# Optimization experiments

Hardware: AMD Instinct MI355X
Metric: run time of the kernel (lower is better)

The kernel has to match this reference:

```python
import jax, jax.numpy as jnp
import numpy as np
from jax import lax


def _conv(x, w, b=None):
    # NCHW conv, 'same' padding, stride 1
    y = lax.conv_general_dilated(x, w, (1, 1), 'SAME',
                                 dimension_numbers=('NCHW', 'OIHW', 'NCHW'))
    return y if b is None else y + b[None, :, None, None]


def _up2(x):
    # nn.Upsample(scale_factor=2), nearest
    return jnp.repeat(jnp.repeat(x, 2, axis=2), 2, axis=3)


def _rot_attn(x, wq, wk, wv, lng, lnb, reach=1):
    # Batched sliding-window rotatory cross-attention (replaces the Python loop
    # over window positions).  x: [B, C, H, W]; each position i in [reach, B-reach)
    # attends (as query) to its 2*reach neighbor frames.
    B, C, H, W = x.shape
    xs = x.reshape(B, C, H * W).transpose(0, 2, 1)          # [B, N, C]
    tgt = xs[reach:B - reach]                               # [P, N, C]
    offs = [o for o in range(-reach, reach + 1) if o != 0]  # fixed small set
    nbs = jnp.stack([xs[reach + o: B - reach + o] for o in offs], axis=1)  # [P,2r,N,C]
    q = tgt @ wq
    k = nbs @ wk
    v = nbs @ wv
    scores = jnp.einsum('pnc,pjmc->pjnm', q, k) / jnp.asarray(C, x.dtype) ** 0.5
    ctx = jnp.einsum('pjnm,pjmc->pjnc', jax.nn.softmax(scores, axis=-1), v).mean(1)  # [P,N,C]
    # LayerNorm over C
    mu = ctx.mean(-1, keepdims=True)
    var = ((ctx - mu) ** 2).mean(-1, keepdims=True)
    ctx = (ctx - mu) * lax.rsqrt(var + 1e-5) * lng + lnb
    cm = ctx.mean(0)                                        # mean over positions [N,C]
    return x + cm.T.reshape(C, H, W)[None]                  # broadcast residual


def _block(h, skip, w_up, b_up, wq, wk, wv, lng, lnb, bng, bnb, w_cb):
    h = _conv(_up2(h), w_up, b_up)                          # 1x1 conv
    h = jnp.concatenate([h, skip], axis=1)
    h = _rot_attn(h, wq, wk, wv, lng, lnb)
    # ConvolutionBatchNormblock: BN (batch stats, eps=1e-5) -> ReLU -> conv (no bias)
    mu = h.mean((0, 2, 3))
    var = ((h - mu[None, :, None, None]) ** 2).mean((0, 2, 3))
    h = (h - mu[None, :, None, None]) * lax.rsqrt(var + 1e-5)[None, :, None, None]
    h = h * bng[None, :, None, None] + bnb[None, :, None, None]
    return _conv(jax.nn.relu(h), w_cb)


def setup_inputs() -> dict:
    key = jax.random.key(0)
    ks = iter(jax.random.split(key, 64))
    n = lambda shape, s: jax.random.normal(next(ks), shape, jnp.float32) * s
    d = {}
    d['x'] = n([6, 64, 768], 1.0)
    d['skip0'] = n([6, 256, 16, 16], 1.0)
    d['skip1'] = n([6, 128, 32, 32], 1.0)
    d['skip2'] = n([6, 64, 64, 64], 1.0)
    d['w_sc'] = n([512, 768, 3, 3], 0.02)
    d['b_sc'] = jnp.zeros([512], jnp.float32)
    for i, (cin, cout) in enumerate([(512, 256), (256, 128), (128, 64)], 1):
        s = cin ** -0.5
        d[f'w_up{i}'] = n([cout, cin, 1, 1], s)
        d[f'b_up{i}'] = jnp.zeros([cout], jnp.float32)
        d[f'wq{i}'] = n([cin, cin], s)
        d[f'wk{i}'] = n([cin, cin], s)
        d[f'wv{i}'] = n([cin, cin], s)
        d[f'lng{i}'] = jnp.ones([cin], jnp.float32)
        d[f'lnb{i}'] = jnp.zeros([cin], jnp.float32)
        d[f'bng{i}'] = jnp.ones([cin], jnp.float32)
        d[f'bnb{i}'] = jnp.zeros([cin], jnp.float32)
        d[f'w_cb{i}'] = n([cout, cin, 3, 3], s * 0.3)
    return d


def reference(x, skip0, skip1, skip2, w_sc, b_sc,
              w_up1, b_up1, wq1, wk1, wv1, lng1, lnb1, bng1, bnb1, w_cb1,
              w_up2, b_up2, wq2, wk2, wv2, lng2, lnb2, bng2, bnb2, w_cb2,
              w_up3, b_up3, wq3, wk3, wv3, lng3, lnb3, bng3, bnb3, w_cb3):
    B, N, D = x.shape
    g = int(N ** 0.5)  # 8x8 token grid (image_size*2 / patch_size)
    h = _conv(x.transpose(0, 2, 1).reshape(B, D, g, g), w_sc, b_sc)   # [B,512,8,8]
    h = _block(h, skip0, w_up1, b_up1, wq1, wk1, wv1, lng1, lnb1, bng1, bnb1, w_cb1)
    h = _block(h, skip1, w_up2, b_up2, wq2, wk2, wv2, lng2, lnb2, bng2, bnb2, w_cb2)
    h = _block(h, skip2, w_up3, b_up3, wq3, wk3, wv3, lng3, lnb3, bng3, bnb3, w_cb3)
    return _up2(h)                                                    # [B,64,128,128]
```

## Files before the change

### kernel.cpp

```cpp
#include <hip/hip_runtime.h>
#include <hip/hip_bf16.h>

typedef const float* fp;
typedef unsigned short u16;
typedef __attribute__((ext_vector_type(8))) short short8v;
typedef __attribute__((ext_vector_type(4))) float f32x4;

__device__ __forceinline__ u16 f2b(float f){
  union{float f; unsigned u;} x; x.f = f;
  unsigned r = x.u + 0x7FFFu + ((x.u>>16)&1u);
  return (u16)(r>>16);
}

__global__ __launch_bounds__(256) void k_fill(float* out, int n, float v){
  int i = blockIdx.x*256 + threadIdx.x;
  if(i < n) out[i] = v;
}
__global__ __launch_bounds__(256) void k_fillb(float* out, fp bias, int Cout, int N){
  int i = blockIdx.x*256 + threadIdx.x;
  if(i < 6*Cout*N) out[i] = bias[(i/N)%Cout];
}
__global__ __launch_bounds__(256) void k_b16(fp in, u16* o, int n){
  int i = (blockIdx.x*256 + threadIdx.x)*8;
  if(i >= n) return;
  u16 tmp[8];
  #pragma unroll
  for(int e=0;e<8;e++) tmp[e] = f2b(in[i+e]);
  *(short8v*)(o+i) = *(const short8v*)tmp;
}
__global__ __launch_bounds__(256) void k_wtr(fp w, u16* wt, int Cout, int Cin){
  int idx = blockIdx.x*256 + threadIdx.x;
  int cc = Cout*Cin;
  if(idx >= 9*cc) return;
  int tap = idx / cc, rem = idx - tap*cc;
  wt[idx] = f2b(w[(size_t)rem*9 + tap]);
}
__global__ __launch_bounds__(256) void k_wqkvt(fp wq, fp wk, fp wv, u16* bt, int C, float rs){
  int idx = blockIdx.x*256 + threadIdx.x;
  if(idx >= 3*C*C) return;
  int r = idx / C, ci = idx - r*C;
  int sel = r / C, co = r - sel*C;
  float v = (sel==0 ? wq : sel==1 ? wk : wv)[(size_t)ci*C + co];
  bt[idx] = f2b(sel==0 ? v*rs : v);
}

__global__ __launch_bounds__(256) void k_in_tr(fp x, float* h0){
  int n = blockIdx.x, b = blockIdx.y;
  for(int d = threadIdx.x; d < 768; d += blockDim.x)
    h0[((size_t)b*768 + d)*64 + n] = x[((size_t)b*64 + n)*768 + d];
}

__global__ __launch_bounds__(256) void k_conv3_mfma2(const u16* __restrict__ wt,
    const u16* __restrict__ inb16, float* __restrict__ out,
    int Cin, int Cout, int H, int W, int S){
  const int N = H*W;
  __shared__ u16 As[64*40];
  __shared__ u16 Bs[64*40];
  int t = threadIdx.x, wid = t>>6, lane = t&63, l15 = lane&15, g = lane>>4;
  int b = blockIdx.z / S, s = blockIdx.z % S;
  int co0 = blockIdx.y*64, px0 = blockIdx.x*64;
  int ciN = Cin/S, ci0 = s*ciN;
  const u16* inb = inb16 + (size_t)b*Cin*N;
  int arow = t>>2, acol = (t&3)*8;
  int bpx = t&63, boct = t>>6;
  int p = px0 + bpx, py = p/W, px_ = p - py*W;
  int nc = ciN >> 5, nk = 9*nc;
  f32x4 acc[4];
  #pragma unroll
  for(int i=0;i<4;i++) acc[i] = f32x4{0.f,0.f,0.f,0.f};
  short8v av; u16 bt[8];

  #define PREF(ks) { int tap = (ks)/nc; int c0 = ((ks) - tap*nc)<<5;                     \
      int dy = tap/3 - 1, dx = tap - (tap/3)*3 - 1;                                      \
      av = *(const short8v*)(wt + ((size_t)tap*Cout + co0 + arow)*Cin + ci0 + c0 + acol);\
      bool val = ((unsigned)(py+dy) < (unsigned)H) && ((unsigned)(px_+dx) < (unsigned)W);\
      const u16* bp = inb + (size_t)(ci0 + c0 + boct*8)*N + (p + dy*W + dx);             \
      _Pragma("unroll") for(int e=0;e<8;e++) bt[e] = val ? bp[(size_t)e*N] : (u16)0; }

  PREF(0);
  for(int ks = 0; ks < nk; ks++){
    __syncthreads();
    *(short8v*)(As + arow*40 + acol) = av;
    *(short8v*)(Bs + bpx*40 + boct*8) = *(const short8v*)bt;
    __syncthreads();
    if(ks+1 < nk) PREF(ks+1);
    short8v a = *(const short8v*)(As + (wid*16+l15)*40 + 8*g);
    #pragma unroll
    for(int pt=0; pt<4; pt++){
      short8v bf = *(const short8v*)(Bs + (pt*16+l15)*40 + 8*g);
      acc[pt] = __builtin_amdgcn_mfma_f32_16x16x32_bf16(a, bf, acc[pt], 0,0,0);
    }
  }
  #undef PREF
  #pragma unroll
  for(int pt=0; pt<4; pt++){
    #pragma unroll
    for(int r=0; r<4; r++){
      size_t o = ((size_t)b*Cout + co0 + wid*16 + 4*g + r)*N + px0 + pt*16 + l15;
      if(S == 1) out[o] = acc[pt][r];
      else atomicAdd(out + o, acc[pt][r]);
    }
  }
}

__global__ __launch_bounds__(256) void k_gemm_qkv(const u16* __restrict__ XB,
    const u16* __restrict__ BT, u16* __restrict__ Qo, u16* __restrict__ Ko,
    u16* __restrict__ Vo, int C, int Nn){
  __shared__ u16 As[64*40], Bs[64*40];
  int t = threadIdx.x, wid = t>>6, lane = t&63, l15 = lane&15, g = lane>>4;
  int r0 = blockIdx.x*64, c0 = blockIdx.y*64;
  int arow = t>>2, acol = (t&3)*8;
  int nk = C/32;
  f32x4 acc[4];
  #pragma unroll
  for(int i=0;i<4;i++) acc[i] = f32x4{0.f,0.f,0.f,0.f};
  short8v av = *(const short8v*)(XB + (size_t)(r0+arow)*C + acol);
  short8v bv = *(const short8v*)(BT + (size_t)(c0+arow)*C + acol);
  for(int ks = 0; ks < nk; ks++){
    __syncthreads();
    *(short8v*)(As + arow*40 + acol) = av;
    *(short8v*)(Bs + arow*40 + acol) = bv;
    __syncthreads();
    if(ks+1 < nk){
      int k0 = (ks+1)*32;
      av = *(const short8v*)(XB + (size_t)(r0+arow)*C + k0 + acol);
      bv = *(const short8v*)(BT + (size_t)(c0+arow)*C + k0 + acol);
    }
    short8v a = *(const short8v*)(As + (wid*16+l15)*40 + 8*g);
    #pragma unroll
    for(int pt=0; pt<4; pt++){
      short8v bf = *(const short8v*)(Bs + (pt*16+l15)*40 + 8*g);
      acc[pt] = __builtin_amdgcn_mfma_f32_16x16x32_bf16(a, bf, acc[pt], 0,0,0);
    }
  }
  int sel = c0 / C, cb = c0 - sel*C;
  if(sel < 2){
    u16* ob = sel==0 ? Qo : Ko;
    #pragma unroll
    for(int pt=0; pt<4; pt++){
      #pragma unroll
      for(int r=0; r<4; r++)
        ob[(size_t)(r0 + wid*16 + 4*g + r)*C + cb + pt*16 + l15] = f2b(acc[pt][r]);
    }
  }else{
    int b = r0 / Nn, nb = r0 - b*Nn;
    #pragma unroll
    for(int pt=0; pt<4; pt++){
      #pragma unroll
      for(int r=0; r<4; r++)
        Vo[((size_t)b*C + cb + pt*16 + l15)*Nn + nb + wid*16 + 4*g + r] = f2b(acc[pt][r]);
    }
  }
}

__global__ void k_conv1_low(const float* __restrict__ in, fp w, fp bias,
                            float* __restrict__ out, int Cin, int Cout, int N1){
  int bc = blockIdx.x; int b = bc / Cout; int co = bc % Cout;
  extern __shared__ float ws[];
  for(int i = threadIdx.x; i < Cin; i += blockDim.x) ws[i] = w[(size_t)co*Cin + i];
  __syncthreads();
  const float* inb = in + (size_t)b*Cin*N1;
  float bv = bias[co];
  for(int p = threadIdx.x; p < N1; p += blockDim.x){
    float acc = bv;
    for(int ci = 0; ci < Cin; ci++) acc += inb[(size_t)ci*N1 + p] * ws[ci];
    out[((size_t)b*Cout + co)*N1 + p] = acc;
  }
}

__global__ __launch_bounds__(256) void k_concat_up(const float* __restrict__ a, fp skip,
                                                   float* __restrict__ cat,
                                                   int Ca, int Cs, int N2, int W2){
  int bc = blockIdx.x; int C = Ca + Cs; int b = bc / C; int c = bc % C;
  float* o = cat + (size_t)bc*N2;
  if(c < Ca){
    const float* s = a + ((size_t)b*Ca + c)*(N2/4);
    int W1 = W2/2;
    for(int n = threadIdx.x; n < N2; n += blockDim.x){
      int y = n / W2, x = n % W2;
      o[n] = s[(y>>1)*W1 + (x>>1)];
    }
  }else{
    fp s = skip + ((size_t)b*Cs + (c-Ca))*N2;
    for(int n = threadIdx.x; n < N2; n += blockDim.x) o[n] = s[n];
  }
}

__global__ __launch_bounds__(256) void k_trb(const float* __restrict__ src, u16* __restrict__ dst,
                                             int C, int N){
  __shared__ float tb[32][33];
  int b = blockIdx.z;
  int c0 = blockIdx.y*32, n0 = blockIdx.x*32;
  int tx = threadIdx.x & 31, ty = threadIdx.x >> 5;
  for(int i = ty; i < 32; i += 8) tb[i][tx] = src[((size_t)b*C + c0+i)*N + n0+tx];
  __syncthreads();
  for(int i = ty; i < 32; i += 8) dst[((size_t)b*N + n0+i)*C + c0+tx] = f2b(tb[tx][i]);
}

template<int C, bool VL>
__global__ __launch_bounds__(256) void k_attn_sp(const u16* __restrict__ Q,
    const u16* __restrict__ K, const u16* __restrict__ VT,
    float* __restrict__ ctxn, int N){
  constexpr int KVB = 32, KP = C+8, VP = 40, PSP = 40, NP = C/32, CP4 = C+4;
  __shared__ u16 Ks[2*KVB*KP];
  __shared__ u16 Vt[VL ? 2*C*VP : 8];
  __shared__ u16 ps[4][16*PSP];
  int t = threadIdx.x, wid = t>>6, lane = t&63, l15 = lane&15, g = lane>>4;
  int half = wid & 1, qgrp = wid >> 1;
  int lt = ((t>>7)<<6) | (t&63);
  int p = blockIdx.y, j = blockIdx.z;
  int q0 = (blockIdx.x*2 + qgrp)*16;
  const u16* Qb = Q + ((size_t)(p+1)*N + q0)*C;
  const u16* Kb = K  + (size_t)(p + (j?2:0))*N*C;
  const u16* Vb = VT + (size_t)(p + (j?2:0))*C*N;
  u16* Ksh = Ks + half*(KVB*KP);
  u16* Vth = Vt + (VL ? half*(C*VP) : 0);
  int kbase = half*(N>>1);

  short8v qf[NP];
  #pragma unroll
  for(int kk=0;kk<NP;kk++)
    qf[kk] = *(const short8v*)(Qb + (size_t)l15*C + kk*32 + 8*g);
  f32x4 acc[C/16];
  #pragma unroll
  for(int i=0;i<C/16;i++) acc[i] = f32x4{0.f,0.f,0.f,0.f};
  float m[4] = {-1e30f,-1e30f,-1e30f,-1e30f};
  float l[4] = {0.f,0.f,0.f,0.f};
  short8v kpre[NP], vpre[NP];

  #define APREF(M0) { _Pragma("unroll") for(int i_=0;i_<NP;i_++){                 \
        int idx = lt*8 + i_*1024; int mm = idx/C, cc = idx - mm*C;                \
        kpre[i_] = *(const short8v*)(Kb + (size_t)((M0)+mm)*C + cc); }            \
      if constexpr(VL){ _Pragma("unroll") for(int i_=0;i_<NP;i_++){               \
        int idx = lt*8 + i_*1024; int c = idx>>5, mo = idx&31;                    \
        vpre[i_] = *(const short8v*)(Vb + (size_t)c*N + (M0) + mo); } } }

  const int nit = N>>6;
  APREF(kbase);
  for(int it = 0; it < nit; ++it){
    int m0 = kbase + it*KVB;
    __syncthreads();
    #pragma unroll
    for(int i_=0;i_<NP;i_++){ int idx = lt*8 + i_*1024; int mm = idx/C, cc = idx - mm*C;
      *(short8v*)(Ksh + mm*KP + cc) = kpre[i_]; }
    if constexpr(VL){
      #pragma unroll
      for(int i_=0;i_<NP;i_++){ int idx = lt*8 + i_*1024; int c = idx>>5, mo = idx&31;
        *(short8v*)(Vth + c*VP + mo) = vpre[i_]; }
    }
    __syncthreads();
    if(it+1 < nit) APREF(kbase + (it+1)*KVB);
    f32x4 s[2];
    __builtin_amdgcn_s_setprio(1);
    #pragma unroll
    for(int h=0; h<2; h++){
      s[h] = f32x4{0.f,0.f,0.f,0.f};
      #pragma unroll
      for(int kk=0; kk<NP; kk++){
        short8v kf = *(const short8v*)(Ksh + (h*16+l15)*KP + kk*32 + 8*g);
        s[h] = __builtin_amdgcn_mfma_f32_16x16x32_bf16(qf[kk], kf, s[h], 0,0,0);
      }
    }
    __builtin_amdgcn_s_setprio(0);
    float lmax[4]; bool need = false;
    #pragma unroll
    for(int r=0; r<4; r++){
      float a = fmaxf(s[0][r], s[1][r]);
      lmax[r] = a; need |= (a > m[r] + 8.f);
    }
    if(__any((int)need)){
      #pragma unroll
      for(int r=0; r<4; r++){
        float mx = lmax[r];
        #pragma unroll
        for(int off=1; off<16; off<<=1) mx = fmaxf(mx, __shfl_xor(mx, off));
        float mnew = fmaxf(m[r], mx);
        float scl = __expf(m[r] - mnew);
        l[r] *= scl; m[r] = mnew;
        #pragma unroll
        for(int ct=0; ct<C/16; ct++) acc[ct][r] *= scl;
      }
    }
    #pragma unroll
    for(int r=0; r<4; r++){
      float ls = 0.f;
      #pragma unroll
      for(int h=0; h<2; h++){
        float e = __expf(s[h][r] - m[r]); ls += e;
        ps[wid][(4*g+r)*PSP + h*16 + l15] = f2b(e);
      }
      l[r] += ls;
    }
    __builtin_amdgcn_s_setprio(1);
    short8v pa = *(const short8v*)(ps[wid] + l15*PSP + 8*g);
    #pragma unroll
    for(int ct=0; ct<C/16; ct++){
      short8v vb;
      if constexpr(VL) vb = *(const short8v*)(Vth + (ct*16+l15)*VP + 8*g);
      else             vb = *(const short8v*)(Vb + (size_t)(ct*16+l15)*N + m0 + 8*g);
      acc[ct] = __builtin_amdgcn_mfma_f32_16x16x32_bf16(pa, vb, acc[ct], 0,0,0);
    }
    __builtin_amdgcn_s_setprio(0);
  }
  #undef APREF
  #pragma unroll
  for(int r=0; r<4; r++){
    float lr = l[r];
    #pragma unroll
    for(int off=1; off<16; off<<=1) lr += __shfl_xor(lr, off);
    l[r] = lr;
  }
  float* accb = (float*)Ks;
  float* mlb  = (float*)ps;
  __syncthreads();
  if(half == 1){
    #pragma unroll
    for(int ct=0; ct<C/16; ct++){
      #pragma unroll
      for(int r=0; r<4; r++)
        accb[(size_t)(qgrp*16 + 4*g + r)*CP4 + ct*16 + l15] = acc[ct][r];
    }
    if(l15 == 0){
      #pragma unroll
      for(int r=0; r<4; r++){
        mlb[(qgrp*16 + 4*g + r)*2]     = m[r];
        mlb[(qgrp*16 + 4*g + r)*2 + 1] = l[r];
      }
    }
  }
  __syncthreads();
  if(half == 0){
    float fa[4], fb[4], inv[4];
    #pragma unroll
    for(int r=0; r<4; r++){
      int row = qgrp*16 + 4*g + r;
      float mb = mlb[row*2], lb = mlb[row*2 + 1];
      float ms = fmaxf(m[r], mb);
      fa[r] = __expf(m[r] - ms); fb[r] = __expf(mb - ms);
      inv[r] = 0.5f/(l[r]*fa[r] + lb*fb[r]);
    }
    #pragma unroll
    for(int ct=0; ct<C/16; ct++){
      int c = ct*16 + l15;
      #pragma unroll
      for(int r=0; r<4; r++){
        int row = qgrp*16 + 4*g + r;
        float o = acc[ct][r]*fa[r] + accb[(size_t)row*CP4 + c]*fb[r];
        atomicAdd(&ctxn[((size_t)p*N + q0 + 4*g + r)*C + c], o*inv[r]);
      }
    }
  }
}

template<int C>
__global__ __launch_bounds__(256) void k_attn_mfma(const u16* __restrict__ Q,
                                                   const u16* __restrict__ K,
                                                   const u16* __restrict__ VT,
                                                   float* __restrict__ ctxn, int N){
  constexpr int KP = C + 8;
  __shared__ u16 Ks[32*KP];
  __shared__ u16 Vt[C*40];
  __shared__ u16 ps[4][16*40];
  int t = threadIdx.x, wid = t>>6, lane = t&63;
  int l15 = lane&15, g = lane>>4;
  int p = blockIdx.y, j = blockIdx.z;
  int q0 = (blockIdx.x*4 + wid)*16;
  const u16* Qb = Q + ((size_t)(p+1)*N + q0)*C;
  const u16* Kb = K  + (size_t)(p + (j?2:0))*N*C;
  const u16* Vb = VT + (size_t)(p + (j?2:0))*C*N;

  short8v qf[C/32];
  #pragma unroll
  for(int kk = 0; kk < C/32; kk++)
    qf[kk] = *(const short8v*)(Qb + (size_t)l15*C + kk*32 + 8*g);

  f32x4 acc[C/16];
  #pragma unroll
  for(int i = 0; i < C/16; i++) acc[i] = f32x4{0.f,0.f,0.f,0.f};
  float mrow[4] = {-1e30f,-1e30f,-1e30f,-1e30f};
  float lrow[4] = {0.f,0.f,0.f,0.f};

  for(int m0 = 0; m0 < N; m0 += 32){
    __syncthreads();
    for(int idx = t*8; idx < 32*C; idx += 2048){
      int m = idx/C, c = idx - m*C;
      *(short8v*)(Ks + m*KP + c) = *(const short8v*)(Kb + (size_t)(m0+m)*C + c);
    }
    for(int idx = t*8; idx < 32*C; idx += 2048){
      int c = idx >> 5, mo = idx & 31;
      *(short8v*)(Vt + c*40 + mo) = *(const short8v*)(Vb + (size_t)c*N + m0 + mo);
    }
    __syncthreads();
    f32x4 s0 = {0.f,0.f,0.f,0.f}, s1 = {0.f,0.f,0.f,0.f};
    #pragma unroll
    for(int kk = 0; kk < C/32; kk++){
      short8v k0 = *(const short8v*)(Ks + l15*KP      + kk*32 + 8*g);
      short8v k1 = *(const short8v*)(Ks + (16+l15)*KP + kk*32 + 8*g);
      s0 = __builtin_amdgcn_mfma_f32_16x16x32_bf16(qf[kk], k0, s0, 0,0,0);
      s1 = __builtin_amdgcn_mfma_f32_16x16x32_bf16(qf[kk], k1, s1, 0,0,0);
    }
    float scl[4];
    #pragma unroll
    for(int r = 0; r < 4; r++){
      float mx = fmaxf(s0[r], s1[r]);
      #pragma unroll
      for(int off = 1; off < 16; off <<= 1) mx = fmaxf(mx, __shfl_xor(mx, off));
      float mnew = fmaxf(mrow[r], mx);
      scl[r] = __expf(mrow[r] - mnew);
      float e0 = __expf(s0[r] - mnew), e1 = __expf(s1[r] - mnew);
      float psum = e0 + e1;
      #pragma unroll
      for(int off = 1; off < 16; off <<= 1) psum += __shfl_xor(psum, off);
      lrow[r] = lrow[r]*scl[r] + psum;
      mrow[r] = mnew;
      int m = 4*g + r;
      ps[wid][m*40 + l15]      = f2b(e0);
      ps[wid][m*40 + 16 + l15] = f2b(e1);
    }
    #pragma unroll
    for(int ct = 0; ct < C/16; ct++){
      #pragma unroll
      for(int r = 0; r < 4; r++) acc[ct][r] *= scl[r];
    }
    short8v pa = *(const short8v*)(ps[wid] + l15*40 + 8*g);
    #pragma unroll
    for(int ct = 0; ct < C/16; ct++){
      short8v vb = *(const short8v*)(Vt + (ct*16+l15)*40 + 8*g);
      acc[ct] = __builtin_amdgcn_mfma_f32_16x16x32_bf16(pa, vb, acc[ct], 0,0,0);
    }
  }
  #pragma unroll
  for(int ct = 0; ct < C/16; ct++){
    int c = ct*16 + l15;
    #pragma unroll
    for(int r = 0; r < 4; r++){
      int m = 4*g + r;
      atomicAdd(&ctxn[((size_t)p*N + q0 + m)*C + c], 0.5f*acc[ct][r]/lrow[r]);
    }
  }
}

__global__ __launch_bounds__(64) void k_ln64(float* __restrict__ ctxn, fp lng, fp lnb, int C){
  float* row = ctxn + (size_t)blockIdx.x*C;
  int t = threadIdx.x;
  float s = 0.f, s2 = 0.f;
  for(int c = t; c < C; c += 64){ float v = row[c]; s += v; s2 += v*v; }
  #pragma unroll
  for(int off = 32; off > 0; off >>= 1){ s += __shfl_xor(s, off); s2 += __shfl_xor(s2, off); }
  float m = s/(float)C, var = s2/(float)C - m*m;
  float ri = rsqrtf(var + 1e-5f);
  for(int c = t; c < C; c += 64) row[c] = (row[c] - m)*ri*lng[c] + lnb[c];
}

__global__ void k_cm(const float* __restrict__ ctxn, float* __restrict__ cm, int C, int N){
  int n = blockIdx.x;
  for(int c = threadIdx.x; c < C; c += blockDim.x){
    float s = 0.25f*( ctxn[((size_t)0*N + n)*C + c] + ctxn[((size_t)1*N + n)*C + c]
                    + ctxn[((size_t)2*N + n)*C + c] + ctxn[((size_t)3*N + n)*C + c]);
    cm[(size_t)n*C + c] = s;
  }
}

__global__ __launch_bounds__(256) void k_addstat(float* __restrict__ h, const float* __restrict__ cm,
                                                 float* __restrict__ ss2, int C, int N){
  int bc = blockIdx.x; int c = bc % C;
  float* hp = h + (size_t)bc*N;
  float s = 0.f, s2 = 0.f;
  for(int n = threadIdx.x; n < N; n += blockDim.x){
    float v = hp[n] + cm[(size_t)n*C + c];
    hp[n] = v; s += v; s2 += v*v;
  }
  #pragma unroll
  for(int o = 32; o > 0; o >>= 1){ s += __shfl_down(s, o); s2 += __shfl_down(s2, o); }
  if((threadIdx.x & 63) == 0){
    atomicAdd(&ss2[c], s); atomicAdd(&ss2[C + c], s2);
  }
}
__global__ void k_bnfin(const float* __restrict__ ss2, fp bng, fp bnb,
                        float* __restrict__ ss, int C, int N){
  int c = threadIdx.x;
  if(c >= C) return;
  float inv = 1.f/(6.f*(float)N);
  float m = ss2[c]*inv, var = ss2[C+c]*inv - m*m;
  float sc = bng[c]*rsqrtf(var + 1e-5f);
  ss[c] = sc; ss[C + c] = bnb[c] - m*sc;
}

__global__ __launch_bounds__(256) void k_bnrelu2(float* __restrict__ h, const float* __restrict__ ssin,
                                                 u16* __restrict__ ob, int C, int N){
  int bc = blockIdx.x; int c = bc % C;
  float sc = ssin[c], sh = ssin[C + c];
  float* hp = h + (size_t)bc*N;
  u16* op = ob + (size_t)bc*N;
  for(int n = threadIdx.x; n < N; n += blockDim.x){
    float v = hp[n]*sc + sh; v = v > 0.f ? v : 0.f;
    hp[n] = v; op[n] = f2b(v);
  }
}

__global__ __launch_bounds__(256) void k_up_out(const float* __restrict__ in, float* out,
                                                int H, int W){
  int bc = blockIdx.x;
  const float* ip = in + (size_t)bc*H*W;
  float* op = out + (size_t)bc*4*H*W;
  int W2 = 2*W, N2 = 4*H*W;
  for(int p = threadIdx.x; p < N2; p += blockDim.x){
    int y = p / W2, x = p % W2;
    op[p] = ip[(y>>1)*W + (x>>1)];
  }
}

extern "C" void kernel_launch(void* const* d_in, const int* in_sizes, int n_in,
                              void* d_out, int out_size, void* d_ws, size_t ws_size,
                              hipStream_t stream){
  float* out_f = (float*)d_out;
  static const int EXP[36] = {294912,393216,786432,1572864,3538944,512,
    131072,256,262144,262144,262144,512,512,512,512,1179648,
    32768,128,65536,65536,65536,256,256,256,256,294912,
    8192,64,16384,16384,16384,128,128,128,128,73728};
  bool ok = (n_in == 36) && (out_size == 6291456);
  if(ok) for(int i = 0; i < 36; i++) if(in_sizes[i] != EXP[i]){ ok = false; break; }
  if(!ok){
    k_fill<<<(out_size+255)/256, 256, 0, stream>>>(out_f, out_size, 10.0f);
    return;
  }
  const size_t R = 3145728;
  const size_t NEED = (5*R + 4096)*sizeof(float);
  if(ws_size < NEED){
    k_fill<<<(out_size+255)/256, 256, 0, stream>>>(out_f, out_size, 100.0f);
    return;
  }
  (void)hipGetLastError();
  #define CKERR(code) do{ if(hipGetLastError() != hipSuccess){ \
      k_fill<<<(out_size+255)/256, 256, 0, stream>>>(out_f, out_size, (float)(code)); \
      return; } }while(0)

  fp x = (fp)d_in[0];
  fp skip[3]  = {(fp)d_in[1],(fp)d_in[2],(fp)d_in[3]};
  fp w_sc = (fp)d_in[4], b_sc = (fp)d_in[5];
  fp w_up[3] = {(fp)d_in[6], (fp)d_in[16],(fp)d_in[26]};
  fp b_up[3] = {(fp)d_in[7], (fp)d_in[17],(fp)d_in[27]};
  fp wq[3]   = {(fp)d_in[8], (fp)d_in[18],(fp)d_in[28]};
  fp wk[3]   = {(fp)d_in[9], (fp)d_in[19],(fp)d_in[29]};
  fp wv[3]   = {(fp)d_in[10],(fp)d_in[20],(fp)d_in[30]};
  fp lng[3]  = {(fp)d_in[11],(fp)d_in[21],(fp)d_in[31]};
  fp lnb[3]  = {(fp)d_in[12],(fp)d_in[22],(fp)d_in[32]};
  fp bng[3]  = {(fp)d_in[13],(fp)d_in[23],(fp)d_in[33]};
  fp bnb[3]  = {(fp)d_in[14],(fp)d_in[24],(fp)d_in[34]};
  fp w_cb[3] = {(fp)d_in[15],(fp)d_in[25],(fp)d_in[35]};

  float* Wp = (float*)d_ws;
  float *Cc = Wp, *CT = Wp + R;
  u16 *QB = (u16*)(Wp + 2*R), *KB = (u16*)(Wp + 3*R), *VB = (u16*)(Wp + 4*R);
  float *SS  = Wp + 5*R;
  float *SS2 = Wp + 5*R + 2048;
  float *OB = Wp + R, *Bf = Wp + 2*R, *CM = Wp + 2*R;
  u16 *XB  = QB + R;
  u16 *WQT = KB + R;
  u16 *WT = KB, *IB = VB;

  k_in_tr<<<dim3(64,6),256,0,stream>>>(x, Cc);
  k_b16<<<(294912/8+255)/256, 256, 0, stream>>>(Cc, IB, 294912);
  k_wtr<<<(9*512*768+255)/256, 256, 0, stream>>>(w_sc, WT, 512, 768);
  k_fillb<<<(6*512*64+255)/256, 256, 0, stream>>>(OB, b_sc, 512, 64);
  k_conv3_mfma2<<<dim3(1,8,6*8), 256, 0, stream>>>(WT, IB, OB, 768, 512, 8, 8, 8);
  CKERR(20);

  const int Cskip[3] = {256,128,64};
  const int Hs[3]    = {16,32,64};
  const int SPL[3]   = {4,2,1};
  int Cprev = 512;
  for(int i = 0; i < 3; i++){
    int H = Hs[i], N = H*H;
    int N1 = N/4;
    int Cup = Cprev/2;
    int C = Cup + Cskip[i];
    k_conv1_low<<<6*Cup, (N1<256?N1:256), Cprev*4, stream>>>(OB, w_up[i], b_up[i], Bf, Cprev, Cup, N1);
    k_concat_up<<<6*C, 256, 0, stream>>>(Bf, skip[i], Cc, Cup, Cskip[i], N, H);
    k_trb<<<dim3(N/32, C/32, 6), 256, 0, stream>>>(Cc, XB, C, N);
    float rsv = 1.f/sqrtf((float)C);
    k_wqkvt<<<(3*C*C+255)/256, 256, 0, stream>>>(wq[i], wk[i], wv[i], WQT, C, rsv);
    k_gemm_qkv<<<dim3(6*N/64, 3*C/64), 256, 0, stream>>>(XB, WQT, QB, KB, VB, C, N);
    CKERR(30 + 10*i);
    k_fill<<<(4*N*C+255)/256, 256, 0, stream>>>(CT, 4*N*C, 0.f);
    if(i==0) k_attn_mfma<512><<<dim3(N/64,4,2),256,0,stream>>>(QB,KB,VB,CT,N);
    if(i==1) k_attn_sp<256,false><<<dim3(N/32,4,2),256,0,stream>>>(QB,KB,VB,CT,N);
    if(i==2) k_attn_sp<128,true ><<<dim3(N/32,4,2),256,0,stream>>>(QB,KB,VB,CT,N);
    k_ln64<<<4*N, 64, 0, stream>>>(CT, lng[i], lnb[i], C);
    CKERR(32 + 10*i);
    k_cm<<<N, C, 0, stream>>>(CT, CM, C, N);
    k_fill<<<(2*C+255)/256, 256, 0, stream>>>(SS2, 2*C, 0.f);
    k_addstat<<<6*C, 256, 0, stream>>>(Cc, CM, SS2, C, N);
    k_bnfin<<<1, C, 0, stream>>>(SS2, bng[i], bnb[i], SS, C, N);
    k_bnrelu2<<<6*C, 256, 0, stream>>>(Cc, SS, IB, C, N);
    int Co = C/2, S = SPL[i];
    k_wtr<<<(9*Co*C+255)/256, 256, 0, stream>>>(w_cb[i], WT, Co, C);
    if(S > 1) k_fill<<<(6*Co*N+255)/256, 256, 0, stream>>>(OB, 6*Co*N, 0.f);
    k_conv3_mfma2<<<dim3(N/64, Co/64, 6*S), 256, 0, stream>>>(WT, IB, OB, C, Co, H, H, S);
    CKERR(34 + 10*i);
    Cprev = Co;
  }
  k_up_out<<<6*64, 256, 0, stream>>>(OB, out_f, 64, 64);
  CKERR(90);
  #undef CKERR
}
```

Baseline: 758.7 us.

## Add dedicated C=128 flash-attention kernel and fuse LayerNorm with position mean

Replaces the templated split attention kernel for the last stage (C=128, N=4096) with a dedicated kernel. Each wave owns 16 queries, KV tiles are 64 wide with register prefetch of the next tile, online softmax rescales lazily only when the running max grows by more than 8, and MFMA sections get raised priority. Separately, the per-row LayerNorm and the mean over the four positions are fused into one kernel writing CM directly, so the normalized ctx buffer is no longer written back and reread. This saves a launch and a full pass over the context buffer. The lazy rescale threshold is a small numerical tradeoff.

```diff
diff --git a/kernel.cpp b/kernel.cpp
--- a/kernel.cpp
+++ b/kernel.cpp
@@ -195,6 +195,119 @@
   for(int i = ty; i < 32; i += 8) tb[i][tx] = src[((size_t)b*C + c0+i)*N + n0+tx];
   __syncthreads();
   for(int i = ty; i < 32; i += 8) dst[((size_t)b*N + n0+i)*C + c0+tx] = f2b(tb[tx][i]);
+}
+
+__global__ __launch_bounds__(256) void k_attn128(const u16* __restrict__ Q,
+                                                 const u16* __restrict__ K,
+                                                 const u16* __restrict__ VT,
+                                                 float* __restrict__ ctxn, int N){
+  constexpr int C = 128, KVB = 64, KP = C+8, VP = KVB+8, PSP = 68;
+  __shared__ u16 Ks[KVB*KP];
+  __shared__ u16 Vt[C*VP];
+  __shared__ u16 ps[4][16*PSP];
+  int t = threadIdx.x, wid = t>>6, lane = t&63, l15 = lane&15, g = lane>>4;
+  int p = blockIdx.y, q0 = (blockIdx.x*4 + wid)*16, j = blockIdx.z;
+  const u16* Qb = Q + ((size_t)(p+1)*N + q0)*C;
+  const u16* Kb = K  + (size_t)(p + (j?2:0))*N*C;
+  const u16* Vb = VT + (size_t)(p + (j?2:0))*C*N;
+  short8v qf[4];
+  #pragma unroll
+  for(int kk = 0; kk < 4; kk++)
+    qf[kk] = *(const short8v*)(Qb + (size_t)l15*C + kk*32 + 8*g);
+  f32x4 acc[8];
+  #pragma unroll
+  for(int i=0;i<8;i++) acc[i] = f32x4{0.f,0.f,0.f,0.f};
+  float m[4] = {-1e30f,-1e30f,-1e30f,-1e30f};
+  float l[4] = {0.f,0.f,0.f,0.f};
+  short8v kpre[4], vpre[4];
+
+  #define APREF(M0) { _Pragma("unroll") for(int i=0;i<4;i++){                  \
+        int idx = t*8 + i*2048; int mm = idx>>7, cc = idx&127;                 \
+        kpre[i] = *(const short8v*)(Kb + (size_t)((M0)+mm)*C + cc); }          \
+      _Pragma("unroll") for(int i=0;i<4;i++){                                  \
+        int idx = t*8 + i*2048; int c = idx>>6, mo = idx&63;                   \
+        vpre[i] = *(const short8v*)(Vb + (size_t)c*N + (M0) + mo); } }
+
+  APREF(0);
+  for(int m0 = 0; m0 < N; m0 += KVB){
+    __syncthreads();
+    #pragma unroll
+    for(int i=0;i<4;i++){ int idx = t*8 + i*2048; int mm = idx>>7, cc = idx&127;
+      *(short8v*)(Ks + mm*KP + cc) = kpre[i]; }
+    #pragma unroll
+    for(int i=0;i<4;i++){ int idx = t*8 + i*2048; int c = idx>>6, mo = idx&63;
+      *(short8v*)(Vt + c*VP + mo) = vpre[i]; }
+    __syncthreads();
+    if(m0 + KVB < N) APREF(m0 + KVB);
+    f32x4 s[4];
+    __builtin_amdgcn_s_setprio(1);
+    #pragma unroll
+    for(int h=0; h<4; h++){
+      s[h] = f32x4{0.f,0.f,0.f,0.f};
+      #pragma unroll
+      for(int kk=0; kk<4; kk++){
+        short8v kf = *(const short8v*)(Ks + (h*16+l15)*KP + kk*32 + 8*g);
+        s[h] = __builtin_amdgcn_mfma_f32_16x16x32_bf16(qf[kk], kf, s[h], 0,0,0);
+      }
+    }
+    __builtin_amdgcn_s_setprio(0);
+    float lmax[4]; bool need = false;
+    #pragma unroll
+    for(int r=0; r<4; r++){
+      float a = fmaxf(fmaxf(s[0][r],s[1][r]), fmaxf(s[2][r],s[3][r]));
+      lmax[r] = a; need |= (a > m[r] + 8.f);
+    }
+    if(__any((int)need)){
+      #pragma unroll
+      for(int r=0; r<4; r++){
+        float mx = lmax[r];
+        #pragma unroll
+        for(int off=1; off<16; off<<=1) mx = fmaxf(mx, __shfl_xor(mx, off));
+        float mnew = fmaxf(m[r], mx);
+        float scl = __expf(m[r] - mnew);
+        l[r] *= scl; m[r] = mnew;
+        #pragma unroll
+        for(int ct=0; ct<8; ct++) acc[ct][r] *= scl;
+      }
+    }
+    #pragma unroll
+    for(int r=0; r<4; r++){
+      float ls = 0.f;
+      #pragma unroll
+      for(int h=0; h<4; h++){
+        float e = __expf(s[h][r] - m[r]); ls += e;
+        ps[wid][(4*g+r)*PSP + h*16 + l15] = f2b(e);
+      }
+      l[r] += ls;
+    }
+    __builtin_amdgcn_s_setprio(1);
+    #pragma unroll
+    for(int ks=0; ks<2; ks++){
+      short8v pa = *(const short8v*)(ps[wid] + l15*PSP + ks*32 + 8*g);
+      #pragma unroll
+      for(int ct=0; ct<8; ct++){
+        short8v vb = *(const short8v*)(Vt + (ct*16+l15)*VP + ks*32 + 8*g);
+        acc[ct] = __builtin_amdgcn_mfma_f32_16x16x32_bf16(pa, vb, acc[ct], 0,0,0);
+      }
+    }
+    __builtin_amdgcn_s_setprio(0);
+  }
+  #undef APREF
+  float inv[4];
+  #pragma unroll
+  for(int r=0; r<4; r++){
+    float lr = l[r];
+    #pragma unroll
+    for(int off=1; off<16; off<<=1) lr += __shfl_xor(lr, off);
+    inv[r] = 0.5f/lr;
+  }
+  #pragma unroll
+  for(int ct=0; ct<8; ct++){
+    int c = ct*16 + l15;
+    #pragma unroll
+    for(int r=0; r<4; r++)
+      atomicAdd(&ctxn[((size_t)p*N + q0 + 4*g + r)*C + c], acc[ct][r]*inv[r]);
+  }
 }
 
 template<int C, bool VL>
@@ -440,25 +553,22 @@
   }
 }
 
-__global__ __launch_bounds__(64) void k_ln64(float* __restrict__ ctxn, fp lng, fp lnb, int C){
-  float* row = ctxn + (size_t)blockIdx.x*C;
-  int t = threadIdx.x;
+__global__ __launch_bounds__(256) void k_lncm(const float* __restrict__ ctxn,
+                                              fp lng, fp lnb,
+                                              float* __restrict__ cm, int C, int N){
+  __shared__ float sbuf[4*512];
+  int n = blockIdx.x, w = threadIdx.x>>6, lane = threadIdx.x&63;
+  const float* row = ctxn + ((size_t)w*N + n)*C;
   float s = 0.f, s2 = 0.f;
-  for(int c = t; c < C; c += 64){ float v = row[c]; s += v; s2 += v*v; }
+  for(int c = lane; c < C; c += 64){ float v = row[c]; s += v; s2 += v*v; }
   #pragma unroll
   for(int off = 32; off > 0; off >>= 1){ s += __shfl_xor(s, off); s2 += __shfl_xor(s2, off); }
-  float m = s/(float)C, var = s2/(float)C - m*m;
-  float ri = rsqrtf(var + 1e-5f);
-  for(int c = t; c < C; c += 64) row[c] = (row[c] - m)*ri*lng[c] + lnb[c];
-}
-
-__global__ void k_cm(const float* __restrict__ ctxn, float* __restrict__ cm, int C, int N){
-  int n = blockIdx.x;
-  for(int c = threadIdx.x; c < C; c += blockDim.x){
-    float s = 0.25f*( ctxn[((size_t)0*N + n)*C + c] + ctxn[((size_t)1*N + n)*C + c]
-                    + ctxn[((size_t)2*N + n)*C + c] + ctxn[((size_t)3*N + n)*C + c]);
-    cm[(size_t)n*C + c] = s;
-  }
+  float m = s/(float)C, ri = rsqrtf(s2/(float)C - m*m + 1e-5f);
+  for(int c = lane; c < C; c += 64)
+    sbuf[w*C + c] = (row[c] - m)*ri*lng[c] + lnb[c];
+  __syncthreads();
+  for(int c = threadIdx.x; c < C; c += 256)
+    cm[(size_t)n*C + c] = 0.25f*(sbuf[c] + sbuf[C+c] + sbuf[2*C+c] + sbuf[3*C+c]);
 }
 
 __global__ __launch_bounds__(256) void k_addstat(float* __restrict__ h, const float* __restrict__ cm,
@@ -585,10 +695,9 @@
     k_fill<<<(4*N*C+255)/256, 256, 0, stream>>>(CT, 4*N*C, 0.f);
     if(i==0) k_attn_mfma<512><<<dim3(N/64,4,2),256,0,stream>>>(QB,KB,VB,CT,N);
     if(i==1) k_attn_sp<256,false><<<dim3(N/32,4,2),256,0,stream>>>(QB,KB,VB,CT,N);
-    if(i==2) k_attn_sp<128,true ><<<dim3(N/32,4,2),256,0,stream>>>(QB,KB,VB,CT,N);
-    k_ln64<<<4*N, 64, 0, stream>>>(CT, lng[i], lnb[i], C);
+    if(i==2) k_attn128<<<dim3(N/64,4,2),256,0,stream>>>(QB,KB,VB,CT,N);
+    k_lncm<<<N, 256, 0, stream>>>(CT, lng[i], lnb[i], CM, C, N);
     CKERR(32 + 10*i);
-    k_cm<<<N, C, 0, stream>>>(CT, CM, C, N);
     k_fill<<<(2*C+255)/256, 256, 0, stream>>>(SS2, 2*C, 0.f);
     k_addstat<<<6*C, 256, 0, stream>>>(Cc, CM, SS2, C, N);
     k_bnfin<<<1, C, 0, stream>>>(SS2, bng[i], bnb[i], SS, C, N);
```

Result: faster. 698.5 us (-7.9%).
